# Optimization experiments

Hardware: AMD Instinct MI355X
Metric: run time of the kernel (lower is better)

The kernel has to match this reference:

```python
import jax, jax.numpy as jnp
import numpy as np

D = 1024
H = 16
DH = D // H
F = 4096
EPS = 1e-5

def layernorm(x, gamma, beta):
    mean = jnp.mean(x, axis=-1, keepdims=True)
    var = jnp.mean((x - mean) ** 2, axis=-1, keepdims=True)  # biased variance
    return gamma * (x - mean) / jnp.sqrt(var + EPS) + beta

def setup_inputs() -> dict:
    key = jax.random.key(0)
    ks = jax.random.split(key, 12)
    s = 1.0 / np.sqrt(D)
    sf = 1.0 / np.sqrt(F)
    return {
        "x": jax.random.normal(ks[0], (16, 512, D), dtype=jnp.float32),
        "Wq": jax.random.normal(ks[1], (H, D, DH), dtype=jnp.float32) * s,
        "Wk": jax.random.normal(ks[2], (H, D, DH), dtype=jnp.float32) * s,
        "Wv": jax.random.normal(ks[3], (H, D, DH), dtype=jnp.float32) * s,
        "Wo": jax.random.normal(ks[4], (D, D), dtype=jnp.float32) * s,
        "bo": jax.random.normal(ks[5], (D,), dtype=jnp.float32) * s,
        "gamma1": jnp.ones((D,), dtype=jnp.float32),
        "beta1": jnp.zeros((D,), dtype=jnp.float32),
        "gamma2": jnp.ones((D,), dtype=jnp.float32),
        "beta2": jnp.zeros((D,), dtype=jnp.float32),
        "W1": jax.random.normal(ks[6], (D, F), dtype=jnp.float32) * s,
        "b1": jax.random.normal(ks[7], (F,), dtype=jnp.float32) * s,
        "W2": jax.random.normal(ks[8], (F, D), dtype=jnp.float32) * sf,
        "b2": jax.random.normal(ks[9], (D,), dtype=jnp.float32) * sf,
    }

def reference(x, Wq, Wk, Wv, Wo, bo, gamma1, beta1, gamma2, beta2, W1, b1, W2, b2):
    B, S, _ = x.shape
    n1 = layernorm(x, gamma1, beta1)
    # per-head projections (no bias) -> [B,H,S,DH]
    Q = jnp.einsum('bsd,hde->bhse', n1, Wq)
    K = jnp.einsum('bsd,hde->bhse', n1, Wk)
    V = jnp.einsum('bsd,hde->bhse', n1, Wv)
    scores = jnp.einsum('bhse,bhte->bhst', Q, K) / jnp.sqrt(jnp.float32(DH))
    causal = jnp.tril(jnp.ones((S, S), dtype=bool))  # keep lower triangle
    scores = jnp.where(causal, scores, -jnp.inf)
    attn = jax.nn.softmax(scores, axis=-1)  # dropout is identity at eval
    heads = jnp.einsum('bhst,bhte->bhse', attn, V)
    concat = heads.transpose(0, 2, 1, 3).reshape(B, S, D)  # concat heads in order
    x = x + (concat @ Wo + bo)
    n2 = layernorm(x, gamma2, beta2)
    ff = jax.nn.gelu(n2 @ W1 + b1, approximate=False) @ W2 + b2
    return x + ff
```

## Files before the change

### kernel.cpp

```cpp
#include <hip/hip_runtime.h>
#include <hip/hip_bf16.h>
#include <math.h>

constexpr int Dm = 1024;
constexpr int Hh = 16;
constexpr int Ff = 4096;
constexpr int Ss = 512;
constexpr int Bbatch = 16;
constexpr int NT = Bbatch * Ss;
constexpr float EPSc = 1e-5f;

typedef __attribute__((ext_vector_type(8))) short bfrag;
typedef __attribute__((ext_vector_type(4))) float f32x4;

static __device__ __forceinline__ float gelu_f(float v) {
    const float u = v * (0.7978845608f + 0.0356774081f * v * v);
    const float e = __expf(2.0f * u);
    const float th = 1.0f - 2.0f / (e + 1.0f);
    return 0.5f * v * (1.0f + th);
}

static __device__ __forceinline__ void gload16(const void* g, void* l) {
    __builtin_amdgcn_global_load_lds((__attribute__((address_space(1))) void*)g,
                                     (__attribute__((address_space(3))) void*)l,
                                     16, 0, 0);
}

#define SWZ(row, colb) ((row) * 128 + ((colb) ^ (((row) & 7) << 4)))

__global__ void __launch_bounds__(256) transpose_cvt(const float* __restrict__ in,
                                                     __hip_bfloat16* __restrict__ out,
                                                     int R, int C,
                                                     long in_zs, long out_zs) {
    __shared__ float tile[32][33];
    const float* inz = in + (size_t)blockIdx.z * in_zs;
    __hip_bfloat16* outz = out + (size_t)blockIdx.z * out_zs;
    const int c0 = blockIdx.x * 32, r0 = blockIdx.y * 32;
    const int tx = threadIdx.x & 31, ty4 = (threadIdx.x >> 5) * 4;
    #pragma unroll
    for (int i = 0; i < 4; i++)
        tile[ty4 + i][tx] = inz[(size_t)(r0 + ty4 + i) * C + c0 + tx];
    __syncthreads();
    #pragma unroll
    for (int i = 0; i < 4; i++)
        outz[(size_t)(c0 + ty4 + i) * R + r0 + tx] = __float2bfloat16(tile[tx][ty4 + i]);
}

__global__ void __launch_bounds__(256) ln_bf16(const float* __restrict__ x,
                                               const float* __restrict__ gamma,
                                               const float* __restrict__ beta,
                                               __hip_bfloat16* __restrict__ out) {
    const int row = blockIdx.x;
    const int tid = threadIdx.x;
    const int lane = tid & 63, w = tid >> 6;
    float4 xv = reinterpret_cast<const float4*>(x + (size_t)row * Dm)[tid];
    float s  = xv.x + xv.y + xv.z + xv.w;
    float ss = xv.x * xv.x + xv.y * xv.y + xv.z * xv.z + xv.w * xv.w;
    #pragma unroll
    for (int o = 32; o > 0; o >>= 1) {
        s  += __shfl_down(s,  o, 64);
        ss += __shfl_down(ss, o, 64);
    }
    __shared__ float red[2][4];
    if (lane == 0) { red[0][w] = s; red[1][w] = ss; }
    __syncthreads();
    float st  = red[0][0] + red[0][1] + red[0][2] + red[0][3];
    float sst = red[1][0] + red[1][1] + red[1][2] + red[1][3];
    float mean = st * (1.0f / Dm);
    float var  = sst * (1.0f / Dm) - mean * mean;
    float inv  = rsqrtf(var + EPSc);
    float4 g = reinterpret_cast<const float4*>(gamma)[tid];
    float4 b = reinterpret_cast<const float4*>(beta)[tid];
    __hip_bfloat16 t[4] __attribute__((aligned(8)));
    t[0] = __float2bfloat16((xv.x - mean) * inv * g.x + b.x);
    t[1] = __float2bfloat16((xv.y - mean) * inv * g.y + b.y);
    t[2] = __float2bfloat16((xv.z - mean) * inv * g.z + b.z);
    t[3] = __float2bfloat16((xv.w - mean) * inv * g.w + b.w);
    *reinterpret_cast<ushort4*>(out + (size_t)row * Dm + tid * 4) =
        *reinterpret_cast<ushort4*>(t);
}

template<int EPI>
__global__ void __launch_bounds__(256) gemm_db(const __hip_bfloat16* __restrict__ A, int lda,
                                               const __hip_bfloat16* __restrict__ Bt, int ldb,
                                               const float* __restrict__ bias,
                                               const float* __restrict__ res,
                                               void* __restrict__ Cout, int ldc,
                                               int nbx, int K) {
    __shared__ __hip_bfloat16 As[2][128 * 64];
    __shared__ __hip_bfloat16 Bs[2][128 * 64];
    const int tid = threadIdx.x, l = tid & 63, w = tid >> 6;
    const int lr = l & 15, lg = l >> 4;
    const int nwg = gridDim.x;
    const int sbid = (blockIdx.x & 7) * (nwg >> 3) + (blockIdx.x >> 3);
    const int st = sbid >> 6, wi = sbid & 63;
    const int nsx = nbx >> 3;
    const int bx = (st % nsx) * 8 + (wi & 7);
    const int by = (st / nsx) * 8 + (wi >> 3);
    const int m0 = by * 128, n0 = bx * 128;
    const int wr = w >> 1, wc = w & 1;
    const int srow = l >> 3;
    const int scol = ((l & 7) ^ srow) * 8;
    const int NK = K >> 6;

    const __hip_bfloat16* pA  = A  + (size_t)(m0 + w * 32 + srow) * lda + scol;
    const __hip_bfloat16* pBt = Bt + (size_t)(n0 + w * 32 + srow) * ldb + scol;
    auto STAGE = [&](int bsel) {
        #pragma unroll
        for (int j = 0; j < 4; j++) {
            const int rb = w * 32 + j * 8;
            gload16(pA  + (size_t)j * 8 * lda, &As[bsel][rb * 64]);
            gload16(pBt + (size_t)j * 8 * ldb, &Bs[bsel][rb * 64]);
        }
        pA += 64; pBt += 64;
    };

    f32x4 acc[4][4] = {};
    STAGE(0);
    STAGE(1);
    for (int t = 0; t < NK; t++) {
        const int cur = t & 1;
        if (t + 1 < NK) asm volatile("s_waitcnt vmcnt(8)" ::: "memory");
        else            asm volatile("s_waitcnt vmcnt(0)" ::: "memory");
        __builtin_amdgcn_s_barrier();
        __builtin_amdgcn_sched_barrier(0);
        const char* Ab = (const char*)&As[cur][0];
        const char* Bb = (const char*)&Bs[cur][0];
        #pragma unroll
        for (int kk = 0; kk < 2; kk++) {
            bfrag a[4], b[4];
            #pragma unroll
            for (int mi = 0; mi < 4; mi++) {
                const int row = wr * 64 + mi * 16 + lr;
                a[mi] = *(const bfrag*)(Ab + SWZ(row, (kk * 4 + lg) * 16));
            }
            #pragma unroll
            for (int ni = 0; ni < 4; ni++) {
                const int row = wc * 64 + ni * 16 + lr;
                b[ni] = *(const bfrag*)(Bb + SWZ(row, (kk * 4 + lg) * 16));
            }
            __builtin_amdgcn_s_setprio(1);
            #pragma unroll
            for (int mi = 0; mi < 4; mi++)
                #pragma unroll
                for (int ni = 0; ni < 4; ni++)
                    acc[mi][ni] = __builtin_amdgcn_mfma_f32_16x16x32_bf16(a[mi], b[ni], acc[mi][ni], 0, 0, 0);
            __builtin_amdgcn_s_setprio(0);
        }
        __builtin_amdgcn_sched_barrier(0);
        __builtin_amdgcn_s_barrier();
        if (t + 2 < NK) STAGE(cur);
    }
    const int rb = m0 + wr * 64 + lg * 4;
    const int cb = n0 + wc * 64 + lr;
    #pragma unroll
    for (int mi = 0; mi < 4; mi++) {
        #pragma unroll
        for (int ni = 0; ni < 4; ni++) {
            #pragma unroll
            for (int rg = 0; rg < 4; rg++) {
                const int row = rb + mi * 16 + rg;
                const int col = cb + ni * 16;
                const size_t off = (size_t)row * ldc + col;
                const float v = acc[mi][ni][rg];
                if (EPI == 0) {
                    ((__hip_bfloat16*)Cout)[off] = __float2bfloat16(v);
                } else if (EPI == 1) {
                    ((float*)Cout)[off] = v + bias[col] + res[off];
                } else if (EPI == 2) {
                    ((__hip_bfloat16*)Cout)[off] = __float2bfloat16(gelu_f(v + bias[col]));
                } else {
                    ((float*)Cout)[off] = ((float*)Cout)[off] + v + bias[col];
                }
            }
        }
    }
}

__global__ void __launch_bounds__(256) attn_mfma(const __hip_bfloat16* __restrict__ QKV,
                                                 __hip_bfloat16* __restrict__ Oc) {
    constexpr int LDQ = 3072;
    __shared__ __hip_bfloat16 Qs[64 * 64];
    __shared__ __hip_bfloat16 Ks[2][64 * 64];
    __shared__ __hip_bfloat16 Vts[2][64 * 64];
    __shared__ __hip_bfloat16 Ps[4][16 * 64];
    const int tid = threadIdx.x, l = tid & 63, w = tid >> 6;
    const int lr = l & 15, lg = l >> 4;
    const int qt = 7 - (blockIdx.x & 7);
    const int h  = (blockIdx.x >> 3) & 15;
    const int b  = blockIdx.x >> 7;

    const __hip_bfloat16* Qg = QKV + (size_t)(b * Ss + qt * 64) * LDQ + h * 64;
    const __hip_bfloat16* Kg = QKV + (size_t)(b * Ss) * LDQ + 1024 + h * 64;
    const __hip_bfloat16* Vg = QKV + (size_t)(b * Ss) * LDQ + 2048 + h * 64;

    const int r8 = l >> 3;
    const int scol = 8 * ((l & 7) ^ r8);

    const int vkey0 = tid >> 3, vf0 = (tid & 7) * 8;
    const int vkey1 = (tid + 256) >> 3, vf1 = vf0;

    uint4 vr[2];
    auto VLOAD = [&](int kt) {
        vr[0] = *reinterpret_cast<const uint4*>(Vg + (size_t)(kt * 64 + vkey0) * LDQ + vf0);
        vr[1] = *reinterpret_cast<const uint4*>(Vg + (size_t)(kt * 64 + vkey1) * LDQ + vf1);
    };
    auto VWRITE = [&](int bsel) {
        unsigned short* vt = reinterpret_cast<unsigned short*>(Vts[bsel]);
        #pragma unroll
        for (int j = 0; j < 2; j++) {
            const int key = j ? vkey1 : vkey0, f0 = j ? vf1 : vf0;
            const unsigned int rw[4] = {vr[j].x, vr[j].y, vr[j].z, vr[j].w};
            #pragma unroll
            for (int e2 = 0; e2 < 8; e2++) {
                const int feat = f0 + e2;
                const int ad = feat * 128 + ((key * 2) ^ ((feat & 7) << 4));
                vt[ad >> 1] = (unsigned short)(rw[e2 >> 1] >> ((e2 & 1) * 16));
            }
        }
    };
    auto KSTAGE = [&](int kt, int bsel) {
        #pragma unroll
        for (int j = 0; j < 2; j++) {
            const int slot = w * 2 + j;
            gload16(Kg + (size_t)(kt * 64 + slot * 8 + r8) * LDQ + scol,
                    Ks[bsel] + slot * 512);
        }
    };

    #pragma unroll
    for (int j = 0; j < 2; j++) {
        const int slot = w * 2 + j;
        gload16(Qg + (size_t)(slot * 8 + r8) * LDQ + scol, Qs + slot * 512);
    }
    VLOAD(0);
    KSTAGE(0, 0);
    asm volatile("s_waitcnt vmcnt(0)" ::: "memory");
    VWRITE(0);
    asm volatile("s_waitcnt lgkmcnt(0)" ::: "memory");
    __builtin_amdgcn_s_barrier();

    bfrag qf[2];
    #pragma unroll
    for (int kk = 0; kk < 2; kk++)
        qf[kk] = *reinterpret_cast<const bfrag*>(
            (const char*)Qs + SWZ(w * 16 + lr, kk * 64 + lg * 16));

    float m_run[4] = {-1e30f, -1e30f, -1e30f, -1e30f};
    float l_run[4] = {0.f, 0.f, 0.f, 0.f};
    f32x4 acc_o[4] = {};

    for (int kt = 0; kt <= qt; ++kt) {
        const int cur = kt & 1;
        if (kt < qt) {
            VLOAD(kt + 1);
            KSTAGE(kt + 1, cur ^ 1);
            asm volatile("s_waitcnt vmcnt(4)" ::: "memory");
        } else {
            asm volatile("s_waitcnt vmcnt(0)" ::: "memory");
        }
        __builtin_amdgcn_s_barrier();

        f32x4 s4[4] = {};
        #pragma unroll
        for (int kk = 0; kk < 2; kk++) {
            #pragma unroll
            for (int ni = 0; ni < 4; ni++) {
                const bfrag bk = *reinterpret_cast<const bfrag*>(
                    (const char*)Ks[cur] + SWZ(ni * 16 + lr, kk * 64 + lg * 16));
                s4[ni] = __builtin_amdgcn_mfma_f32_16x16x32_bf16(qf[kk], bk, s4[ni], 0, 0, 0);
            }
        }
        float p[4][4];
        #pragma unroll
        for (int ni = 0; ni < 4; ni++)
            #pragma unroll
            for (int rg = 0; rg < 4; rg++)
                p[ni][rg] = s4[ni][rg] * 0.125f;
        if (kt == qt) {
            #pragma unroll
            for (int ni = 0; ni < 4; ni++)
                #pragma unroll
                for (int rg = 0; rg < 4; rg++)
                    if (ni * 16 + lr > w * 16 + lg * 4 + rg) p[ni][rg] = -1e30f;
        }
        float sf[4];
        #pragma unroll
        for (int rg = 0; rg < 4; rg++) {
            float mx = fmaxf(fmaxf(p[0][rg], p[1][rg]), fmaxf(p[2][rg], p[3][rg]));
            #pragma unroll
            for (int o = 1; o < 16; o <<= 1) mx = fmaxf(mx, __shfl_xor(mx, o, 64));
            const float mn = fmaxf(m_run[rg], mx);
            sf[rg] = __expf(m_run[rg] - mn);
            m_run[rg] = mn;
        }
        float rsum[4] = {};
        #pragma unroll
        for (int ni = 0; ni < 4; ni++)
            #pragma unroll
            for (int rg = 0; rg < 4; rg++) {
                const float e = __expf(p[ni][rg] - m_run[rg]);
                p[ni][rg] = e;
                rsum[rg] += e;
            }
        #pragma unroll
        for (int rg = 0; rg < 4; rg++) {
            #pragma unroll
            for (int o = 1; o < 16; o <<= 1) rsum[rg] += __shfl_xor(rsum[rg], o, 64);
            l_run[rg] = l_run[rg] * sf[rg] + rsum[rg];
        }
        #pragma unroll
        for (int di = 0; di < 4; di++)
            #pragma unroll
            for (int rg = 0; rg < 4; rg++)
                acc_o[di][rg] *= sf[rg];

        if (kt < qt) VWRITE(cur ^ 1);

        unsigned short* pw = reinterpret_cast<unsigned short*>(Ps[w]);
        #pragma unroll
        for (int ni = 0; ni < 4; ni++)
            #pragma unroll
            for (int rg = 0; rg < 4; rg++) {
                const int prow = lg * 4 + rg;
                const int ad = SWZ(prow, (ni * 16 + lr) * 2);
                __hip_bfloat16 pb = __float2bfloat16(p[ni][rg]);
                pw[ad >> 1] = *reinterpret_cast<unsigned short*>(&pb);
            }
        #pragma unroll
        for (int kk = 0; kk < 2; kk++) {
            const bfrag pa = *reinterpret_cast<const bfrag*>(
                (const char*)Ps[w] + SWZ(lr, kk * 64 + lg * 16));
            #pragma unroll
            for (int di = 0; di < 4; di++) {
                const bfrag vb = *reinterpret_cast<const bfrag*>(
                    (const char*)Vts[cur] + SWZ(di * 16 + lr, kk * 64 + lg * 16));
                acc_o[di] = __builtin_amdgcn_mfma_f32_16x16x32_bf16(pa, vb, acc_o[di], 0, 0, 0);
            }
        }
        asm volatile("s_waitcnt lgkmcnt(0)" ::: "memory");
        __builtin_amdgcn_s_barrier();
    }
    #pragma unroll
    for (int di = 0; di < 4; di++)
        #pragma unroll
        for (int rg = 0; rg < 4; rg++) {
            const int q = qt * 64 + w * 16 + lg * 4 + rg;
            const float v = acc_o[di][rg] / l_run[rg];
            Oc[(size_t)(b * Ss + q) * Dm + h * 64 + di * 16 + lr] = __float2bfloat16(v);
        }
}

extern "C" void kernel_launch(void* const* d_in, const int* in_sizes, int n_in,
                              void* d_out, int out_size, void* d_ws, size_t ws_size,
                              hipStream_t stream) {
    const float* x   = (const float*)d_in[0];
    const float* Wq  = (const float*)d_in[1];
    const float* Wk  = (const float*)d_in[2];
    const float* Wv  = (const float*)d_in[3];
    const float* Wo  = (const float*)d_in[4];
    const float* bo  = (const float*)d_in[5];
    const float* g1  = (const float*)d_in[6];
    const float* be1 = (const float*)d_in[7];
    const float* g2  = (const float*)d_in[8];
    const float* be2 = (const float*)d_in[9];
    const float* W1  = (const float*)d_in[10];
    const float* b1  = (const float*)d_in[11];
    const float* W2  = (const float*)d_in[12];
    const float* b2  = (const float*)d_in[13];
    float* out = (float*)d_out;

    char* wsb = (char*)d_ws;
    __hip_bfloat16* WqkvT = (__hip_bfloat16*)(wsb);
    __hip_bfloat16* WoT   = (__hip_bfloat16*)(wsb + 6291456);
    __hip_bfloat16* W1T   = (__hip_bfloat16*)(wsb + 8388608);
    __hip_bfloat16* W2T   = (__hip_bfloat16*)(wsb + 16777216);
    __hip_bfloat16* n1    = (__hip_bfloat16*)(wsb + 25165824);
    __hip_bfloat16* QKV   = (__hip_bfloat16*)(wsb + 41943040);
    __hip_bfloat16* concat = n1;
    __hip_bfloat16* n2     = n1;
    __hip_bfloat16* h1     = QKV;

    transpose_cvt<<<dim3(2, 32, 16), 256, 0, stream>>>(Wq, WqkvT,              1024, 64, 65536, 65536);
    transpose_cvt<<<dim3(2, 32, 16), 256, 0, stream>>>(Wk, WqkvT + 1024 * 1024, 1024, 64, 65536, 65536);
    transpose_cvt<<<dim3(2, 32, 16), 256, 0, stream>>>(Wv, WqkvT + 2048 * 1024, 1024, 64, 65536, 65536);
    transpose_cvt<<<dim3(32, 32, 1), 256, 0, stream>>>(Wo, WoT, 1024, 1024, 0, 0);
    transpose_cvt<<<dim3(128, 32, 1), 256, 0, stream>>>(W1, W1T, 1024, 4096, 0, 0);
    transpose_cvt<<<dim3(32, 128, 1), 256, 0, stream>>>(W2, W2T, 4096, 1024, 0, 0);

    ln_bf16<<<NT, 256, 0, stream>>>(x, g1, be1, n1);
    gemm_db<0><<<1536, 256, 0, stream>>>(n1, Dm, WqkvT, Dm, nullptr, nullptr,
                                         QKV, 3072, 24, Dm);
    attn_mfma<<<NT * Hh / 64, 256, 0, stream>>>(QKV, concat);
    gemm_db<1><<<512, 256, 0, stream>>>(concat, Dm, WoT, Dm, bo, x,
                                        out, Dm, 8, Dm);
    ln_bf16<<<NT, 256, 0, stream>>>(out, g2, be2, n2);
    gemm_db<2><<<2048, 256, 0, stream>>>(n2, Dm, W1T, Dm, b1, nullptr,
                                         h1, Ff, 32, Dm);
    gemm_db<3><<<512, 256, 0, stream>>>(h1, Ff, W2T, Ff, b2, nullptr,
                                        out, Dm, 8, Ff);
}
```

Measured before the change: 390.9 us.

## Load GEMM A fragments directly from global memory, stage only B in LDS

The GEMM kernel stops staging the A tile through shared memory. Each wave now loads its A MFMA fragments straight from global memory into registers every K step, and only B keeps the double-buffered LDS path. This halves LDS footprint and LDS traffic per block, which may raise occupancy. The cost is that A loads are now synchronous and unpipelined: they are issued right before the MFMAs with no prefetch. The A tile is also reread by both column waves through the cache instead of being shared via LDS.

```diff
diff --git a/kernel.cpp b/kernel.cpp
--- a/kernel.cpp
+++ b/kernel.cpp
@@ -81,13 +81,12 @@
 }
 
 template<int EPI>
-__global__ void __launch_bounds__(256) gemm_db(const __hip_bfloat16* __restrict__ A, int lda,
+__global__ void __launch_bounds__(256) gemm_ad(const __hip_bfloat16* __restrict__ A, int lda,
                                                const __hip_bfloat16* __restrict__ Bt, int ldb,
                                                const float* __restrict__ bias,
                                                const float* __restrict__ res,
                                                void* __restrict__ Cout, int ldc,
                                                int nbx, int K) {
-    __shared__ __hip_bfloat16 As[2][128 * 64];
     __shared__ __hip_bfloat16 Bs[2][128 * 64];
     const int tid = threadIdx.x, l = tid & 63, w = tid >> 6;
     const int lr = l & 15, lg = l >> 4;
@@ -103,37 +102,35 @@
     const int scol = ((l & 7) ^ srow) * 8;
     const int NK = K >> 6;
 
-    const __hip_bfloat16* pA  = A  + (size_t)(m0 + w * 32 + srow) * lda + scol;
     const __hip_bfloat16* pBt = Bt + (size_t)(n0 + w * 32 + srow) * ldb + scol;
-    auto STAGE = [&](int bsel) {
+    auto STAGEB = [&](int bsel) {
         #pragma unroll
         for (int j = 0; j < 4; j++) {
             const int rb = w * 32 + j * 8;
-            gload16(pA  + (size_t)j * 8 * lda, &As[bsel][rb * 64]);
             gload16(pBt + (size_t)j * 8 * ldb, &Bs[bsel][rb * 64]);
         }
-        pA += 64; pBt += 64;
+        pBt += 64;
     };
+    const __hip_bfloat16* pA = A + (size_t)(m0 + wr * 64 + lr) * lda + lg * 8;
 
     f32x4 acc[4][4] = {};
-    STAGE(0);
-    STAGE(1);
+    STAGEB(0);
+    STAGEB(1);
     for (int t = 0; t < NK; t++) {
         const int cur = t & 1;
-        if (t + 1 < NK) asm volatile("s_waitcnt vmcnt(8)" ::: "memory");
+        if (t + 1 < NK) asm volatile("s_waitcnt vmcnt(4)" ::: "memory");
         else            asm volatile("s_waitcnt vmcnt(0)" ::: "memory");
         __builtin_amdgcn_s_barrier();
-        __builtin_amdgcn_sched_barrier(0);
-        const char* Ab = (const char*)&As[cur][0];
+        bfrag a[4][2];
+        #pragma unroll
+        for (int mi = 0; mi < 4; mi++)
+            #pragma unroll
+            for (int kk = 0; kk < 2; kk++)
+                a[mi][kk] = *(const bfrag*)(pA + (size_t)(mi * 16) * lda + kk * 32);
         const char* Bb = (const char*)&Bs[cur][0];
         #pragma unroll
         for (int kk = 0; kk < 2; kk++) {
-            bfrag a[4], b[4];
-            #pragma unroll
-            for (int mi = 0; mi < 4; mi++) {
-                const int row = wr * 64 + mi * 16 + lr;
-                a[mi] = *(const bfrag*)(Ab + SWZ(row, (kk * 4 + lg) * 16));
-            }
+            bfrag b[4];
             #pragma unroll
             for (int ni = 0; ni < 4; ni++) {
                 const int row = wc * 64 + ni * 16 + lr;
@@ -144,12 +141,13 @@
             for (int mi = 0; mi < 4; mi++)
                 #pragma unroll
                 for (int ni = 0; ni < 4; ni++)
-                    acc[mi][ni] = __builtin_amdgcn_mfma_f32_16x16x32_bf16(a[mi], b[ni], acc[mi][ni], 0, 0, 0);
+                    acc[mi][ni] = __builtin_amdgcn_mfma_f32_16x16x32_bf16(a[mi][kk], b[ni], acc[mi][ni], 0, 0, 0);
             __builtin_amdgcn_s_setprio(0);
         }
         __builtin_amdgcn_sched_barrier(0);
         __builtin_amdgcn_s_barrier();
-        if (t + 2 < NK) STAGE(cur);
+        if (t + 2 < NK) STAGEB(cur);
+        pA += 64;
     }
     const int rb = m0 + wr * 64 + lg * 4;
     const int cb = n0 + wc * 64 + lr;
@@ -389,14 +387,14 @@
     transpose_cvt<<<dim3(32, 128, 1), 256, 0, stream>>>(W2, W2T, 4096, 1024, 0, 0);
 
     ln_bf16<<<NT, 256, 0, stream>>>(x, g1, be1, n1);
-    gemm_db<0><<<1536, 256, 0, stream>>>(n1, Dm, WqkvT, Dm, nullptr, nullptr,
+    gemm_ad<0><<<1536, 256, 0, stream>>>(n1, Dm, WqkvT, Dm, nullptr, nullptr,
                                          QKV, 3072, 24, Dm);
     attn_mfma<<<NT * Hh / 64, 256, 0, stream>>>(QKV, concat);
-    gemm_db<1><<<512, 256, 0, stream>>>(concat, Dm, WoT, Dm, bo, x,
+    gemm_ad<1><<<512, 256, 0, stream>>>(concat, Dm, WoT, Dm, bo, x,
                                         out, Dm, 8, Dm);
     ln_bf16<<<NT, 256, 0, stream>>>(out, g2, be2, n2);
-    gemm_db<2><<<2048, 256, 0, stream>>>(n2, Dm, W1T, Dm, b1, nullptr,
+    gemm_ad<2><<<2048, 256, 0, stream>>>(n2, Dm, W1T, Dm, b1, nullptr,
                                          h1, Ff, 32, Dm);
-    gemm_db<3><<<512, 256, 0, stream>>>(h1, Ff, W2T, Ff, b2, nullptr,
+    gemm_ad<3><<<512, 256, 0, stream>>>(h1, Ff, W2T, Ff, b2, nullptr,
                                         out, Dm, 8, Ff);
 }
```

Result: slower. 581.2 us (+48.7%).
